# Kernel optimization log

Hardware: AMD Instinct MI355X
Metric: run time of the kernel (lower is better)

The kernel has to match this reference:

```python
import jax, jax.numpy as jnp
import numpy as np


def hetcheb(X, src, dst, etype, w, W, b):
    """Heterogeneous Chebyshev graph conv, batched over all (b,t) slices.

    X: [N, BT, C] node features for all batch*time slices at once.
    src/dst/etype/w: [E] edge list with per-edge relation type and weight.
    W: [n_etypes, lk, C, C_out], b: [C_out].
    out = sum_e sum_k T_k(A_e) X @ W[e,k] + b, with T_0=I, T_1=A_e,
          T_k = 2 A_e T_{k-1} - T_{k-2}.
    """
    N = X.shape[0]
    n_etypes, lk = W.shape[0], W.shape[1]
    out = jnp.zeros(X.shape[:2] + (W.shape[-1],), X.dtype)
    for e in range(n_etypes):
        we = jnp.where(etype == e, w, jnp.zeros_like(w))  # mask edges of type e

        def spmm(Z, we=we):
            # A_e @ Z for all BT slices: gather src rows, scale, scatter-add to dst
            return jax.ops.segment_sum(Z[src] * we[:, None, None], dst,
                                       num_segments=N)

        Z0 = X
        out = out + jnp.einsum('nbc,co->nbo', Z0, W[e, 0])
        if lk > 1:
            Z1 = spmm(X)
            out = out + jnp.einsum('nbc,co->nbo', Z1, W[e, 1])
            for k in range(2, lk):
                Z0, Z1 = Z1, 2.0 * spmm(Z1) - Z0
                out = out + jnp.einsum('nbc,co->nbo', Z1, W[e, k])
    return out + b


def reference(x, Wconv, bconv, Wh, bh, Wt, bt,
              hg_src, hg_dst, hg_etype, hg_w,
              tg_src, tg_dst, tg_etype, tg_w):
    kt = Wconv.shape[2]
    c1 = Wconv.shape[0] // 2
    # Temporal GLU conv (Align is identity since c_in == c_out)
    conv = jax.lax.conv_general_dilated(
        x, Wconv, window_strides=(1, 1), padding='VALID',
        dimension_numbers=('NCHW', 'OIHW', 'NCHW')) + bconv[None, :, None, None]
    x_in = x[:, :, kt - 1:, :]
    x_t1 = (conv[:, :c1] + x_in) * jax.nn.sigmoid(conv[:, c1:])  # [B,c1,T,N]

    B, C, T, N = x_t1.shape
    # [B,C,T,N] -> [N, B*T, C]: one batched layout replacing the B*T Python loop
    Xn = x_t1.transpose(3, 0, 2, 1).reshape(N, B * T, C)

    xs = hetcheb(Xn, hg_src, hg_dst, hg_etype, hg_w, Wh, bh)
    xt = hetcheb(Xn, tg_src, tg_dst, tg_etype, tg_w, Wt, bt)

    def back(Z):  # [N, B*T, Co] -> [B, Co, T, N]
        return Z.reshape(N, B, T, -1).transpose(1, 3, 2, 0)

    # Dropout is identity in eval mode
    return jnp.concatenate([back(xs), back(xt)], axis=1)


def setup_inputs() -> dict:
    key = jax.random.key(0)
    ks = jax.random.split(key, 16)
    B, c0, c1, T, N, E, kt, lk, eh, et = 8, 64, 64, 12, 4000, 16000, 3, 3, 3, 2
    x = jax.random.normal(ks[0], (B, c0, T, N), dtype=jnp.float32)
    Wconv = jax.random.normal(ks[1], (2 * c1, c0, kt, 1), dtype=jnp.float32) * 0.05
    bconv = jnp.zeros((2 * c1,), dtype=jnp.float32)
    Wh = jax.random.normal(ks[2], (eh, lk, c1, c1), dtype=jnp.float32) * 0.05
    bh = jnp.zeros((c1,), dtype=jnp.float32)
    Wt = jax.random.normal(ks[3], (et, lk, c1, c1), dtype=jnp.float32) * 0.05
    bt = jnp.zeros((c1,), dtype=jnp.float32)
    hg_src = jax.random.randint(ks[4], (E,), 0, N, dtype=jnp.int32)
    hg_dst = jax.random.randint(ks[5], (E,), 0, N, dtype=jnp.int32)
    hg_etype = jax.random.randint(ks[6], (E,), 0, eh, dtype=jnp.int32)
    hg_w = jax.random.uniform(ks[7], (E,), dtype=jnp.float32)
    tg_src = jax.random.randint(ks[8], (E,), 0, N, dtype=jnp.int32)
    tg_dst = jax.random.randint(ks[9], (E,), 0, N, dtype=jnp.int32)
    tg_etype = jax.random.randint(ks[10], (E,), 0, et, dtype=jnp.int32)
    tg_w = jax.random.uniform(ks[11], (E,), dtype=jnp.float32)
    return {"x": x, "Wconv": Wconv, "bconv": bconv, "Wh": Wh, "bh": bh,
            "Wt": Wt, "bt": bt,
            "hg_src": hg_src, "hg_dst": hg_dst, "hg_etype": hg_etype, "hg_w": hg_w,
            "tg_src": tg_src, "tg_dst": tg_dst, "tg_etype": tg_etype, "tg_w": tg_w}
```

## Files before the change

### kernel.cpp

```cpp
#include <hip/hip_runtime.h>
#include <hip/hip_bf16.h>

typedef __attribute__((ext_vector_type(8))) short short8;
typedef __attribute__((ext_vector_type(4))) float f32x4;

#define B_  8
#define C0  64
#define T_  12
#define TP  10
#define NN  4000
#define CC  64
#define BT  80
#define EE  16000
#define NTILE 63

static __device__ __forceinline__ float bf2f(__hip_bfloat16 h) { return __bfloat162float(h); }
static __device__ __forceinline__ __hip_bfloat16 f2bf(float f) { return __float2bfloat16(f); }

__global__ __launch_bounds__(256) void k_transpose(const float* __restrict__ x,
                                                   __hip_bfloat16* __restrict__ xT) {
  __shared__ __hip_bfloat16 lds[64][72];
  int n0 = blockIdx.x * 64;
  int bt = blockIdx.y; int b = bt / T_, t = bt % T_;
  int tid = threadIdx.x;
#pragma unroll
  for (int i = 0; i < 4; ++i) {
    int vid = tid + i * 256;
    int c = vid >> 4, nv = vid & 15;
    int n = n0 + nv * 4;
    const float* src = x + ((size_t)(b * C0 + c) * T_ + t) * NN;
    float v0 = 0.f, v1 = 0.f, v2 = 0.f, v3 = 0.f;
    if (n + 3 < NN) {
      float4 v = *(const float4*)(src + n);
      v0 = v.x; v1 = v.y; v2 = v.z; v3 = v.w;
    } else {
      if (n     < NN) v0 = src[n];
      if (n + 1 < NN) v1 = src[n + 1];
      if (n + 2 < NN) v2 = src[n + 2];
      if (n + 3 < NN) v3 = src[n + 3];
    }
    lds[nv * 4 + 0][c] = f2bf(v0);
    lds[nv * 4 + 1][c] = f2bf(v1);
    lds[nv * 4 + 2][c] = f2bf(v2);
    lds[nv * 4 + 3][c] = f2bf(v3);
  }
  __syncthreads();
#pragma unroll
  for (int i = 0; i < 2; ++i) {
    int vid = tid + i * 256;
    int nl = vid >> 3, cv = (vid & 7) * 8;
    int n = n0 + nl;
    if (n < NN) {
      short8 v = *(const short8*)(&lds[nl][cv]);
      *(short8*)(xT + ((size_t)(b * T_ + t) * NN + n) * CC + cv) = v;
    }
  }
}

__global__ void k_pack_conv_w(const float* __restrict__ Wc, __hip_bfloat16* __restrict__ wpk) {
  int idx = blockIdx.x * 256 + threadIdx.x;
  if (idx >= 6 * 8 * 64) return;
  int lane = idx & 63, nb = (idx >> 6) & 7, kc = idx >> 9;
  int co = nb * 16 + (lane & 15), quad = lane >> 4;
  __hip_bfloat16* dst = wpk + (size_t)idx * 8;
  for (int j = 0; j < 8; ++j) {
    int k = kc * 32 + quad * 8 + j;
    int dt = k >> 6, ci = k & 63;
    dst[j] = f2bf(Wc[((size_t)co * 64 + ci) * 3 + dt]);
  }
}

__global__ __launch_bounds__(256) void k_conv_glu(const __hip_bfloat16* __restrict__ xT,
                                                  const __hip_bfloat16* __restrict__ wpk,
                                                  const float* __restrict__ bconv,
                                                  __hip_bfloat16* __restrict__ Xn) {
  int lane = threadIdx.x & 63, wv = threadIdx.x >> 6;
  int ntile = blockIdx.x, bt = blockIdx.y;
  int b = bt / TP, t = bt % TP;
  int quad = lane >> 4;
  int arow = ntile * 64 + wv * 16 + (lane & 15);
  if (arow >= NN) arow = NN - 1;
  f32x4 acc[8] = {};
#pragma unroll
  for (int kc = 0; kc < 6; ++kc) {
    int dt = kc >> 1;
    int cb = (kc & 1) * 32 + quad * 8;
    short8 a = *(const short8*)(xT + ((size_t)(b * T_ + t + dt) * NN + arow) * CC + cb);
#pragma unroll
    for (int nb = 0; nb < 8; ++nb) {
      short8 bf = *(const short8*)(wpk + ((size_t)(kc * 8 + nb) * 64 + lane) * 8);
      acc[nb] = __builtin_amdgcn_mfma_f32_16x16x32_bf16(a, bf, acc[nb], 0, 0, 0);
    }
  }
  int row0 = ntile * 64 + wv * 16 + quad * 4;
  if (row0 >= NN) return;
  int col = lane & 15;
  const __hip_bfloat16* xr = xT + ((size_t)(b * T_ + t + 2) * NN) * CC;
#pragma unroll
  for (int nb = 0; nb < 4; ++nb) {
    int co = nb * 16 + col;
    float bP = bconv[co], bQ = bconv[co + 64];
#pragma unroll
    for (int i = 0; i < 4; ++i) {
      float xi = bf2f(xr[(size_t)(row0 + i) * CC + co]);
      float pv = acc[nb][i] + bP + xi;
      float qv = acc[nb + 4][i] + bQ;
      float s = 1.0f / (1.0f + __expf(-qv));
      Xn[((size_t)bt * NN + row0 + i) * CC + co] = f2bf(pv * s);
    }
  }
}

__global__ void k_count(const int* __restrict__ dst, int* __restrict__ cnt) {
  int i = blockIdx.x * 256 + threadIdx.x;
  if (i < EE) atomicAdd(&cnt[dst[i]], 1);
}

__global__ __launch_bounds__(1024) void k_scan(const int* __restrict__ cnt,
                                               int* __restrict__ row_start,
                                               int* __restrict__ cursor) {
  __shared__ int part[1024];
  int tid = threadIdx.x;
  int base = tid * 4;
  int s = 0;
#pragma unroll
  for (int i = 0; i < 4; ++i) { int idx = base + i; if (idx < NN) s += cnt[idx]; }
  part[tid] = s;
  __syncthreads();
  for (int off = 1; off < 1024; off <<= 1) {
    int v = 0;
    if (tid >= off) v = part[tid - off];
    __syncthreads();
    part[tid] += v;
    __syncthreads();
  }
  int run = (tid > 0) ? part[tid - 1] : 0;
#pragma unroll
  for (int i = 0; i < 4; ++i) {
    int idx = base + i;
    if (idx < NN) { row_start[idx] = run; cursor[idx] = run; run += cnt[idx]; }
  }
  if (tid == 1023) row_start[NN] = run;
}

__global__ void k_scatter(const int* __restrict__ src, const int* __restrict__ dst,
                          const int* __restrict__ ety, const float* __restrict__ w,
                          int* __restrict__ cursor, int* __restrict__ es,
                          float* __restrict__ ew, int* __restrict__ et2) {
  int i = blockIdx.x * 256 + threadIdx.x;
  if (i < EE) {
    int p = atomicAdd(&cursor[dst[i]], 1);
    es[p] = src[i]; ew[p] = w[i]; et2[p] = ety[i];
  }
}

struct BPtrs { const __hip_bfloat16* p[3]; };
struct BOut  { __hip_bfloat16* p[3]; };

template <int NE>
__global__ __launch_bounds__(128) void k_spmm(BPtrs in, BOut out,
                                              const int* __restrict__ row_start,
                                              const int* __restrict__ es,
                                              const float* __restrict__ ew,
                                              const int* __restrict__ et2) {
  int lane = threadIdx.x & 63, wv = threadIdx.x >> 6;
  int n = blockIdx.x;
  int btg = blockIdx.y * 2 + wv;
  int bt0 = btg * 8;
  int s0 = row_start[n], s1 = row_start[n + 1];
  float acc[8][NE];
#pragma unroll
  for (int j = 0; j < 8; ++j)
#pragma unroll
    for (int e = 0; e < NE; ++e) acc[j][e] = 0.f;
  for (int i = s0; i < s1; ++i) {
    int s = es[i]; float wgt = ew[i]; int ty = et2[i];
    const __hip_bfloat16* base = in.p[ty] + ((size_t)bt0 * NN + s) * CC + lane;
    float v[8];
#pragma unroll
    for (int j = 0; j < 8; ++j) v[j] = bf2f(base[(size_t)j * NN * CC]);
    float ws[NE];
#pragma unroll
    for (int e = 0; e < NE; ++e) ws[e] = (ty == e) ? wgt : 0.f;
#pragma unroll
    for (int j = 0; j < 8; ++j)
#pragma unroll
      for (int e = 0; e < NE; ++e) acc[j][e] += ws[e] * v[j];
  }
#pragma unroll
  for (int e = 0; e < NE; ++e)
#pragma unroll
    for (int j = 0; j < 8; ++j)
      out.p[e][((size_t)(bt0 + j) * NN + n) * CC + lane] = f2bf(acc[j][e]);
}

__global__ void k_pack_gemm_w(const float* __restrict__ W, __hip_bfloat16* __restrict__ wpk,
                              int NE) {
  int total = (1 + 2 * NE) * 2 * 4 * 64;
  int idx = blockIdx.x * 256 + threadIdx.x;
  if (idx >= total) return;
  int lane = idx & 63, nb = (idx >> 6) & 3, kcg = idx >> 8;
  int kb = kcg >> 1, kc2 = kcg & 1;
  int co = nb * 16 + (lane & 15), quad = lane >> 4;
  __hip_bfloat16* dst = wpk + (size_t)idx * 8;
  for (int j = 0; j < 8; ++j) {
    int c = kc2 * 32 + quad * 8 + j;
    float f;
    if (kb == 0) {
      f = 0.f;
      for (int e = 0; e < NE; ++e)
        f += W[(((size_t)e * 3 + 0) * 64 + c) * 64 + co]
           - W[(((size_t)e * 3 + 2) * 64 + c) * 64 + co];
    } else {
      int e = (kb - 1) >> 1;
      if (kb & 1) f =       W[(((size_t)e * 3 + 1) * 64 + c) * 64 + co];
      else        f = 2.f * W[(((size_t)e * 3 + 2) * 64 + c) * 64 + co];
    }
    dst[j] = f2bf(f);
  }
}

struct ZPtrs { const __hip_bfloat16* p[7]; };

template <int NBLK>
__global__ __launch_bounds__(256) void k_gemm(ZPtrs zs, const __hip_bfloat16* __restrict__ wpk,
                                              const float* __restrict__ bias,
                                              float* __restrict__ out, int choff) {
  int lane = threadIdx.x & 63, wv = threadIdx.x >> 6;
  int ntile = blockIdx.x, bt = blockIdx.y;
  int b = bt / TP, t = bt % TP;
  int quad = lane >> 4;
  int arow = ntile * 64 + wv * 16 + (lane & 15);
  if (arow >= NN) arow = NN - 1;
  f32x4 acc[4] = {};
#pragma unroll
  for (int kb = 0; kb < NBLK; ++kb) {
    const __hip_bfloat16* Z = zs.p[kb];
#pragma unroll
    for (int kc2 = 0; kc2 < 2; ++kc2) {
      short8 a = *(const short8*)(Z + ((size_t)bt * NN + arow) * CC + kc2 * 32 + quad * 8);
#pragma unroll
      for (int nb = 0; nb < 4; ++nb) {
        short8 bf = *(const short8*)(wpk + (((size_t)(kb * 2 + kc2) * 4 + nb) * 64 + lane) * 8);
        acc[nb] = __builtin_amdgcn_mfma_f32_16x16x32_bf16(a, bf, acc[nb], 0, 0, 0);
      }
    }
  }
  int row0 = ntile * 64 + wv * 16 + quad * 4;
  if (row0 >= NN) return;
  int col = lane & 15;
#pragma unroll
  for (int nb = 0; nb < 4; ++nb) {
    int c = nb * 16 + col;
    float bb = bias[c];
    float4 v = make_float4(acc[nb][0] + bb, acc[nb][1] + bb, acc[nb][2] + bb, acc[nb][3] + bb);
    *(float4*)(out + ((size_t)(b * 128 + choff + c) * TP + t) * NN + row0) = v;
  }
}

extern "C" void kernel_launch(void* const* d_in, const int* in_sizes, int n_in,
                              void* d_out, int out_size, void* d_ws, size_t ws_size,
                              hipStream_t stream) {
  const float* x      = (const float*)d_in[0];
  const float* Wconv  = (const float*)d_in[1];
  const float* bconv  = (const float*)d_in[2];
  const float* Wh     = (const float*)d_in[3];
  const float* bh     = (const float*)d_in[4];
  const float* Wt     = (const float*)d_in[5];
  const float* bt_    = (const float*)d_in[6];
  const int*   hg_src = (const int*)d_in[7];
  const int*   hg_dst = (const int*)d_in[8];
  const int*   hg_ety = (const int*)d_in[9];
  const float* hg_w   = (const float*)d_in[10];
  const int*   tg_src = (const int*)d_in[11];
  const int*   tg_dst = (const int*)d_in[12];
  const int*   tg_ety = (const int*)d_in[13];
  const float* tg_w   = (const float*)d_in[14];
  float* out = (float*)d_out;

  char* p = (char*)d_ws;
  auto alloc = [&](size_t bytes) {
    char* r = p;
    p += (bytes + 255) & ~(size_t)255;
    return r;
  };
  const size_t ZN = (size_t)BT * NN * CC;
  __hip_bfloat16* Xn    = (__hip_bfloat16*)alloc(ZN * 2);
  __hip_bfloat16* zbase = (__hip_bfloat16*)alloc(6 * ZN * 2);
  __hip_bfloat16* xT    = (__hip_bfloat16*)alloc((size_t)B_ * T_ * NN * CC * 2);
  __hip_bfloat16* wpkc  = (__hip_bfloat16*)alloc((size_t)6 * 8 * 64 * 8 * 2);
  __hip_bfloat16* wpkg  = (__hip_bfloat16*)alloc((size_t)7 * 2 * 4 * 64 * 8 * 2);
  int*   cnt       = (int*)alloc((size_t)NN * 4);
  int*   row_start = (int*)alloc((size_t)(NN + 1) * 4);
  int*   cursor    = (int*)alloc((size_t)NN * 4);
  int*   es        = (int*)alloc((size_t)EE * 4);
  float* ew        = (float*)alloc((size_t)EE * 4);
  int*   et2       = (int*)alloc((size_t)EE * 4);

  hipLaunchKernelGGL(k_transpose, dim3(NTILE, B_ * T_), dim3(256), 0, stream, x, xT);
  hipLaunchKernelGGL(k_pack_conv_w, dim3(12), dim3(256), 0, stream, Wconv, wpkc);
  hipLaunchKernelGGL(k_conv_glu, dim3(NTILE, BT), dim3(256), 0, stream, xT, wpkc, bconv, Xn);

  for (int g = 0; g < 2; ++g) {
    const int*   gsrc = g ? tg_src : hg_src;
    const int*   gdst = g ? tg_dst : hg_dst;
    const int*   gety = g ? tg_ety : hg_ety;
    const float* gw   = g ? tg_w : hg_w;
    const float* W    = g ? Wt : Wh;
    const float* bias = g ? bt_ : bh;
    int NE = g ? 2 : 3;
    int choff = g ? 64 : 0;

    hipMemsetAsync(cnt, 0, (size_t)NN * 4, stream);
    hipLaunchKernelGGL(k_count, dim3((EE + 255) / 256), dim3(256), 0, stream, gdst, cnt);
    hipLaunchKernelGGL(k_scan, dim3(1), dim3(1024), 0, stream, cnt, row_start, cursor);
    hipLaunchKernelGGL(k_scatter, dim3((EE + 255) / 256), dim3(256), 0, stream,
                       gsrc, gdst, gety, gw, cursor, es, ew, et2);

    BPtrs in1; BOut o1;
    for (int e = 0; e < 3; ++e) { in1.p[e] = Xn; o1.p[e] = zbase + (size_t)(2 * e) * ZN; }
    if (NE == 3)
      hipLaunchKernelGGL(k_spmm<3>, dim3(NN, 5), dim3(128), 0, stream, in1, o1, row_start, es, ew, et2);
    else
      hipLaunchKernelGGL(k_spmm<2>, dim3(NN, 5), dim3(128), 0, stream, in1, o1, row_start, es, ew, et2);

    BPtrs in2; BOut o2;
    for (int e = 0; e < 3; ++e) {
      in2.p[e] = zbase + (size_t)(2 * e) * ZN;
      o2.p[e]  = zbase + (size_t)(2 * e + 1) * ZN;
    }
    if (NE == 3)
      hipLaunchKernelGGL(k_spmm<3>, dim3(NN, 5), dim3(128), 0, stream, in2, o2, row_start, es, ew, et2);
    else
      hipLaunchKernelGGL(k_spmm<2>, dim3(NN, 5), dim3(128), 0, stream, in2, o2, row_start, es, ew, et2);

    int total = (1 + 2 * NE) * 2 * 4 * 64;
    hipLaunchKernelGGL(k_pack_gemm_w, dim3((total + 255) / 256), dim3(256), 0, stream, W, wpkg, NE);

    ZPtrs zs;
    zs.p[0] = Xn;
    for (int k = 1; k < 7; ++k) zs.p[k] = zbase + (size_t)(k - 1) * ZN;
    if (NE == 3)
      hipLaunchKernelGGL(k_gemm<7>, dim3(NTILE, BT), dim3(256), 0, stream, zs, wpkg, bias, out, choff);
    else
      hipLaunchKernelGGL(k_gemm<5>, dim3(NTILE, BT), dim3(256), 0, stream, zs, wpkg, bias, out, choff);
  }
}
```

Before: 689.5 us.

## Stage packed weights in LDS and give each wave four row tiles

The conv-GLU and Chebyshev output GEMM kernels now copy the packed bf16 weight fragments into shared memory once per block. Each wave processes 64 rows (four 16-row MFMA tiles) instead of 16, so every weight fragment is reused across four MFMAs, and the grid shrinks to 16 row-blocks per slice. The aim is to cut redundant global/L2 weight loads and amortise per-block setup, at the cost of more accumulator registers, a larger LDS footprint and fewer blocks in flight.

```diff
diff --git a/kernel.cpp b/kernel.cpp
--- a/kernel.cpp
+++ b/kernel.cpp
@@ -13,6 +13,7 @@
 #define BT  80
 #define EE  16000
 #define NTILE 63
+#define MTILE 16
 
 static __device__ __forceinline__ float bf2f(__hip_bfloat16 h) { return __bfloat162float(h); }
 static __device__ __forceinline__ __hip_bfloat16 f2bf(float f) { return __float2bfloat16(f); }
@@ -70,43 +71,57 @@
   }
 }
 
-__global__ __launch_bounds__(256) void k_conv_glu(const __hip_bfloat16* __restrict__ xT,
-                                                  const __hip_bfloat16* __restrict__ wpk,
-                                                  const float* __restrict__ bconv,
-                                                  __hip_bfloat16* __restrict__ Xn) {
+__global__ __launch_bounds__(256, 2) void k_conv_glu(const __hip_bfloat16* __restrict__ xT,
+                                                     const short8* __restrict__ wpk,
+                                                     const float* __restrict__ bconv,
+                                                     __hip_bfloat16* __restrict__ Xn) {
+  __shared__ short8 bsh[48 * 64];
   int lane = threadIdx.x & 63, wv = threadIdx.x >> 6;
-  int ntile = blockIdx.x, bt = blockIdx.y;
+  int base = blockIdx.x * 256, bt = blockIdx.y;
   int b = bt / TP, t = bt % TP;
-  int quad = lane >> 4;
-  int arow = ntile * 64 + wv * 16 + (lane & 15);
-  if (arow >= NN) arow = NN - 1;
-  f32x4 acc[8] = {};
+  int quad = lane >> 4, col = lane & 15;
+  for (int s = wv; s < 48; s += 4) bsh[s * 64 + lane] = wpk[s * 64 + lane];
+  __syncthreads();
+  int arow[4];
+#pragma unroll
+  for (int rg = 0; rg < 4; ++rg) {
+    int r = base + wv * 64 + rg * 16 + col;
+    arow[rg] = (r < NN) ? r : NN - 1;
+  }
+  f32x4 acc[4][8] = {};
 #pragma unroll
   for (int kc = 0; kc < 6; ++kc) {
     int dt = kc >> 1;
     int cb = (kc & 1) * 32 + quad * 8;
-    short8 a = *(const short8*)(xT + ((size_t)(b * T_ + t + dt) * NN + arow) * CC + cb);
+    const __hip_bfloat16* Zs = xT + ((size_t)(b * T_ + t + dt) * NN) * CC + cb;
+    short8 a[4];
+#pragma unroll
+    for (int rg = 0; rg < 4; ++rg) a[rg] = *(const short8*)(Zs + (size_t)arow[rg] * CC);
 #pragma unroll
     for (int nb = 0; nb < 8; ++nb) {
-      short8 bf = *(const short8*)(wpk + ((size_t)(kc * 8 + nb) * 64 + lane) * 8);
-      acc[nb] = __builtin_amdgcn_mfma_f32_16x16x32_bf16(a, bf, acc[nb], 0, 0, 0);
-    }
-  }
-  int row0 = ntile * 64 + wv * 16 + quad * 4;
-  if (row0 >= NN) return;
-  int col = lane & 15;
+      short8 bf = bsh[(kc * 8 + nb) * 64 + lane];
+#pragma unroll
+      for (int rg = 0; rg < 4; ++rg)
+        acc[rg][nb] = __builtin_amdgcn_mfma_f32_16x16x32_bf16(a[rg], bf, acc[rg][nb], 0, 0, 0);
+    }
+  }
   const __hip_bfloat16* xr = xT + ((size_t)(b * T_ + t + 2) * NN) * CC;
 #pragma unroll
-  for (int nb = 0; nb < 4; ++nb) {
-    int co = nb * 16 + col;
-    float bP = bconv[co], bQ = bconv[co + 64];
-#pragma unroll
-    for (int i = 0; i < 4; ++i) {
-      float xi = bf2f(xr[(size_t)(row0 + i) * CC + co]);
-      float pv = acc[nb][i] + bP + xi;
-      float qv = acc[nb + 4][i] + bQ;
-      float s = 1.0f / (1.0f + __expf(-qv));
-      Xn[((size_t)bt * NN + row0 + i) * CC + co] = f2bf(pv * s);
+  for (int rg = 0; rg < 4; ++rg) {
+    int row0 = base + wv * 64 + rg * 16 + quad * 4;
+    if (row0 >= NN) continue;
+#pragma unroll
+    for (int nb = 0; nb < 4; ++nb) {
+      int co = nb * 16 + col;
+      float bP = bconv[co], bQ = bconv[co + 64];
+#pragma unroll
+      for (int i = 0; i < 4; ++i) {
+        float xi = bf2f(xr[(size_t)(row0 + i) * CC + co]);
+        float pv = acc[rg][nb][i] + bP + xi;
+        float qv = acc[rg][nb + 4][i] + bQ;
+        float s = 1.0f / (1.0f + __expf(-qv));
+        Xn[((size_t)bt * NN + row0 + i) * CC + co] = f2bf(pv * s);
+      }
     }
   }
 }
@@ -223,38 +238,53 @@
 struct ZPtrs { const __hip_bfloat16* p[7]; };
 
 template <int NBLK>
-__global__ __launch_bounds__(256) void k_gemm(ZPtrs zs, const __hip_bfloat16* __restrict__ wpk,
-                                              const float* __restrict__ bias,
-                                              float* __restrict__ out, int choff) {
+__global__ __launch_bounds__(256, 2) void k_gemm(ZPtrs zs, const short8* __restrict__ wpk,
+                                                 const float* __restrict__ bias,
+                                                 float* __restrict__ out, int choff) {
+  __shared__ short8 bsh[NBLK * 8 * 64];
   int lane = threadIdx.x & 63, wv = threadIdx.x >> 6;
-  int ntile = blockIdx.x, bt = blockIdx.y;
+  int base = blockIdx.x * 256, bt = blockIdx.y;
   int b = bt / TP, t = bt % TP;
-  int quad = lane >> 4;
-  int arow = ntile * 64 + wv * 16 + (lane & 15);
-  if (arow >= NN) arow = NN - 1;
-  f32x4 acc[4] = {};
+  int quad = lane >> 4, col = lane & 15;
+  for (int s = wv; s < NBLK * 8; s += 4) bsh[s * 64 + lane] = wpk[s * 64 + lane];
+  __syncthreads();
+  int arow[4];
+#pragma unroll
+  for (int rg = 0; rg < 4; ++rg) {
+    int r = base + wv * 64 + rg * 16 + col;
+    arow[rg] = (r < NN) ? r : NN - 1;
+  }
+  f32x4 acc[4][4] = {};
 #pragma unroll
   for (int kb = 0; kb < NBLK; ++kb) {
-    const __hip_bfloat16* Z = zs.p[kb];
+    const __hip_bfloat16* Z = zs.p[kb] + (size_t)bt * NN * CC;
 #pragma unroll
     for (int kc2 = 0; kc2 < 2; ++kc2) {
-      short8 a = *(const short8*)(Z + ((size_t)bt * NN + arow) * CC + kc2 * 32 + quad * 8);
+      int cb = kc2 * 32 + quad * 8;
+      short8 a[4];
+#pragma unroll
+      for (int rg = 0; rg < 4; ++rg) a[rg] = *(const short8*)(Z + (size_t)arow[rg] * CC + cb);
 #pragma unroll
       for (int nb = 0; nb < 4; ++nb) {
-        short8 bf = *(const short8*)(wpk + (((size_t)(kb * 2 + kc2) * 4 + nb) * 64 + lane) * 8);
-        acc[nb] = __builtin_amdgcn_mfma_f32_16x16x32_bf16(a, bf, acc[nb], 0, 0, 0);
+        short8 bf = bsh[((kb * 2 + kc2) * 4 + nb) * 64 + lane];
+#pragma unroll
+        for (int rg = 0; rg < 4; ++rg)
+          acc[rg][nb] = __builtin_amdgcn_mfma_f32_16x16x32_bf16(a[rg], bf, acc[rg][nb], 0, 0, 0);
       }
     }
   }
-  int row0 = ntile * 64 + wv * 16 + quad * 4;
-  if (row0 >= NN) return;
-  int col = lane & 15;
-#pragma unroll
-  for (int nb = 0; nb < 4; ++nb) {
-    int c = nb * 16 + col;
-    float bb = bias[c];
-    float4 v = make_float4(acc[nb][0] + bb, acc[nb][1] + bb, acc[nb][2] + bb, acc[nb][3] + bb);
-    *(float4*)(out + ((size_t)(b * 128 + choff + c) * TP + t) * NN + row0) = v;
+#pragma unroll
+  for (int rg = 0; rg < 4; ++rg) {
+    int row0 = base + wv * 64 + rg * 16 + quad * 4;
+    if (row0 >= NN) continue;
+#pragma unroll
+    for (int nb = 0; nb < 4; ++nb) {
+      int c = nb * 16 + col;
+      float bb = bias[c];
+      float4 v = make_float4(acc[rg][nb][0] + bb, acc[rg][nb][1] + bb,
+                             acc[rg][nb][2] + bb, acc[rg][nb][3] + bb);
+      *(float4*)(out + ((size_t)(b * 128 + choff + c) * TP + t) * NN + row0) = v;
+    }
   }
 }
 
@@ -299,7 +329,8 @@
 
   hipLaunchKernelGGL(k_transpose, dim3(NTILE, B_ * T_), dim3(256), 0, stream, x, xT);
   hipLaunchKernelGGL(k_pack_conv_w, dim3(12), dim3(256), 0, stream, Wconv, wpkc);
-  hipLaunchKernelGGL(k_conv_glu, dim3(NTILE, BT), dim3(256), 0, stream, xT, wpkc, bconv, Xn);
+  hipLaunchKernelGGL(k_conv_glu, dim3(MTILE, BT), dim3(256), 0, stream,
+                     xT, (const short8*)wpkc, bconv, Xn);
 
   for (int g = 0; g < 2; ++g) {
     const int*   gsrc = g ? tg_src : hg_src;
@@ -341,8 +372,10 @@
     zs.p[0] = Xn;
     for (int k = 1; k < 7; ++k) zs.p[k] = zbase + (size_t)(k - 1) * ZN;
     if (NE == 3)
-      hipLaunchKernelGGL(k_gemm<7>, dim3(NTILE, BT), dim3(256), 0, stream, zs, wpkg, bias, out, choff);
+      hipLaunchKernelGGL(k_gemm<7>, dim3(MTILE, BT), dim3(256), 0, stream,
+                         zs, (const short8*)wpkg, bias, out, choff);
     else
-      hipLaunchKernelGGL(k_gemm<5>, dim3(NTILE, BT), dim3(256), 0, stream, zs, wpkg, bias, out, choff);
-  }
-}
+      hipLaunchKernelGGL(k_gemm<5>, dim3(MTILE, BT), dim3(256), 0, stream,
+                         zs, (const short8*)wpkg, bias, out, choff);
+  }
+}
```

Result: faster. 656.8 us (-4.7%).
